# Optimization experiments

Measured on AMD Instinct MI355X. Metric: run time of the kernel, lower is better.

Reference implementation:

```python
import jax, jax.numpy as jnp
import numpy as np

HEADS = 12
DIM_HEAD = 64

def setup_inputs() -> dict:
    key = jax.random.key(0)
    ks = jax.random.split(key, 5)
    B, S, D = 4, 2048, 768
    s = 0.02
    return {
        "x": jax.random.normal(ks[0], (B, S, D), dtype=jnp.float32),
        "Wq": jax.random.normal(ks[1], (D, D), dtype=jnp.float32) * s,
        "Wk": jax.random.normal(ks[2], (D, D), dtype=jnp.float32) * s,
        "Wv": jax.random.normal(ks[3], (D, D), dtype=jnp.float32) * s,
        "Wo": jax.random.normal(ks[4], (D, D), dtype=jnp.float32) * s,
        "bo": jnp.zeros((D,), dtype=jnp.float32),
    }

def reference(x, Wq, Wk, Wv, Wo, bo):
    B, S, D = x.shape
    H, Dh = HEADS, DIM_HEAD
    scale = Dh ** -0.5
    # projections (torch Linear: x @ W^T)
    q = (x @ Wq.T).reshape(B, S, H, Dh).transpose(0, 2, 1, 3) * scale  # [B,H,S,Dh]
    k = (x @ Wk.T).reshape(B, S, H, Dh).transpose(0, 2, 1, 3)
    v = (x @ Wv.T).reshape(B, S, H, Dh).transpose(0, 2, 1, 3)
    sim = jnp.einsum("bhid,bhjd->bhij", q, k)  # [B,H,S,S]
    mask_value = -jnp.finfo(sim.dtype).max
    causal_mask = jnp.triu(jnp.ones((S, S), dtype=bool), k=1)
    sim = jnp.where(causal_mask, mask_value, sim)
    attn = jax.nn.softmax(sim, axis=-1)
    # dropout is identity in eval mode
    out = jnp.einsum("bhij,bhjd->bhid", attn, v)  # [B,H,S,Dh]
    out = out.transpose(0, 2, 1, 3).reshape(B, S, H * Dh)
    return out @ Wo.T + bo
```

## Files before the change

kernel.cpp:

```cpp
#include <hip/hip_runtime.h>
#include <stdint.h>

typedef unsigned short u16;
typedef __bf16 bf16x8 __attribute__((ext_vector_type(8)));
typedef float f32x4 __attribute__((ext_vector_type(4)));
typedef u16 u16x4 __attribute__((ext_vector_type(4)));
typedef u16 u16x8 __attribute__((ext_vector_type(8)));
typedef uint32_t u32x2 __attribute__((ext_vector_type(2)));

#define LDS_CAST(p) (reinterpret_cast<__attribute__((address_space(3))) uint32_t*>(reinterpret_cast<uintptr_t>(p)))
#define GLB_CAST(p) (reinterpret_cast<const __attribute__((address_space(1))) uint32_t*>(reinterpret_cast<uintptr_t>(p)))
#define GLOAD16(g, l) __builtin_amdgcn_global_load_lds(GLB_CAST(g), LDS_CAST(l), 16, 0, 0)
#define AS3U16(p) (reinterpret_cast<__attribute__((address_space(3))) u16*>(reinterpret_cast<uintptr_t>(p)))

__device__ __forceinline__ u16 f2bf(float f) {
    uint32_t u = __builtin_bit_cast(uint32_t, f);
    u += 0x7fffu + ((u >> 16) & 1u);
    return (u16)(u >> 16);
}
__device__ __forceinline__ u16 bfbits(float f) {
    return __builtin_bit_cast(u16, (__bf16)f);
}

__global__ void cast_all(const float* __restrict__ x,
                         const float* __restrict__ a, const float* __restrict__ b,
                         const float* __restrict__ c, const float* __restrict__ d,
                         u16* __restrict__ ox, u16* __restrict__ oa, u16* __restrict__ ob,
                         u16* __restrict__ oc, u16* __restrict__ od) {
    const int bid = blockIdx.x;
    const float* in;
    u16* out;
    int i;
    if (bid < 6144) {
        in = x; out = ox; i = bid * 256 + threadIdx.x;
    } else {
        const int zb = bid - 6144;
        const int z = zb / 576, lb = zb % 576;
        in = (z == 0) ? a : (z == 1) ? b : (z == 2) ? c : d;
        out = (z == 0) ? oa : (z == 1) ? ob : (z == 2) ? oc : od;
        i = lb * 256 + threadIdx.x;
    }
    float4 f = reinterpret_cast<const float4*>(in)[i];
    u16x4 o;
    o.x = f2bf(f.x); o.y = f2bf(f.y); o.z = f2bf(f.z); o.w = f2bf(f.w);
    reinterpret_cast<u16x4*>(out)[i] = o;
}

__global__ __launch_bounds__(256, 2) void gemm_qkv(
    const u16* __restrict__ X, const u16* __restrict__ Wq,
    const u16* __restrict__ Wk, const u16* __restrict__ Wv,
    u16* __restrict__ qo, u16* __restrict__ ko, u16* __restrict__ vTo)
{
    __shared__ u16 As[2][128 * 32];
    __shared__ u16 Bs[3][2][128 * 32];
    const int tid = threadIdx.x;
    const int lane = tid & 63;
    const int w = tid >> 6;
    const int lr = lane & 15, lg = lane >> 4;
    const int wrow = (w >> 1) * 64, wcol = (w & 1) * 64;

    const int lin = blockIdx.x + blockIdx.y * 6;
    const int xcd = lin & 7, idx = lin >> 3;
    const int prow = xcd * 8 + idx / 6;
    const int bxc = idx % 6;
    const int row0 = prow * 128, col0 = bxc * 128;

    f32x4 acc[3][4][4];
#pragma unroll
    for (int zz = 0; zz < 3; ++zz)
#pragma unroll
        for (int m = 0; m < 4; ++m)
#pragma unroll
            for (int n = 0; n < 4; ++n)
#pragma unroll
                for (int j = 0; j < 4; ++j) acc[zz][m][n][j] = 0.f;

#define QSTAGE(KT)                                                                                 \
    {                                                                                              \
        const int buf_ = (KT) & 1;                                                                 \
        _Pragma("unroll")                                                                          \
        for (int it = 0; it < 2; ++it) {                                                           \
            const int c = it * 256 + w * 64 + lane;                                                \
            const int row = c >> 2, c16 = c & 3;                                                   \
            const size_t go = (size_t)row * 768 + (KT) * 32 + c16 * 8;                             \
            const int lo = (it * 256 + w * 64) * 8;                                                \
            GLOAD16(X  + (size_t)row0 * 768 + go, &As[buf_][lo]);                                  \
            GLOAD16(Wq + (size_t)col0 * 768 + go, &Bs[0][buf_][lo]);                               \
            GLOAD16(Wk + (size_t)col0 * 768 + go, &Bs[1][buf_][lo]);                               \
            GLOAD16(Wv + (size_t)col0 * 768 + go, &Bs[2][buf_][lo]);                               \
        }                                                                                          \
    }

#define QSTEP(KT, VN, PF)                                                                          \
    {                                                                                              \
        if (PF) QSTAGE((KT) + 1);                                                                  \
        asm volatile("s_waitcnt vmcnt(" #VN ")" ::: "memory");                                     \
        __builtin_amdgcn_s_barrier();                                                              \
        const int cur_ = (KT) & 1;                                                                 \
        bf16x8 af[4];                                                                              \
        _Pragma("unroll")                                                                          \
        for (int m = 0; m < 4; ++m) af[m] = *(const bf16x8*)&As[cur_][(wrow + m * 16 + lr) * 32 + lg * 8]; \
        _Pragma("unroll")                                                                          \
        for (int zz = 0; zz < 3; ++zz) {                                                           \
            bf16x8 bfr[4];                                                                         \
            _Pragma("unroll")                                                                      \
            for (int n = 0; n < 4; ++n) bfr[n] = *(const bf16x8*)&Bs[zz][cur_][(wcol + n * 16 + lr) * 32 + lg * 8]; \
            _Pragma("unroll")                                                                      \
            for (int m = 0; m < 4; ++m)                                                            \
                _Pragma("unroll")                                                                  \
                for (int n = 0; n < 4; ++n)                                                        \
                    acc[zz][m][n] = __builtin_amdgcn_mfma_f32_16x16x32_bf16(af[m], bfr[n], acc[zz][m][n], 0, 0, 0); \
        }                                                                                          \
        asm volatile("s_waitcnt lgkmcnt(0)" ::: "memory");                                         \
        __builtin_amdgcn_sched_barrier(0);                                                         \
        __builtin_amdgcn_s_barrier();                                                              \
    }

    QSTAGE(0);
    for (int kt = 0; kt < 23; ++kt) QSTEP(kt, 8, true);
    QSTEP(23, 0, false);
#undef QSTEP
#undef QSTAGE

#pragma unroll
    for (int zz = 0; zz < 2; ++zz) {
        u16* outp = (zz == 0) ? qo : ko;
        const float scl = (zz == 0) ? 0.18033688011112042f : 1.0f;
#pragma unroll
        for (int n = 0; n < 4; ++n) {
            const int j = col0 + wcol + n * 16 + lr;
            const int h = j >> 6, dh = j & 63;
#pragma unroll
            for (int m = 0; m < 4; ++m)
#pragma unroll
                for (int r = 0; r < 4; ++r) {
                    const int i = row0 + wrow + m * 16 + lg * 4 + r;
                    const int b = i >> 11, s = i & 2047;
                    outp[(((size_t)b * 12 + h) * 2048 + s) * 64 + dh] = bfbits(acc[zz][m][n][r] * scl);
                }
        }
    }
    {
#pragma unroll
        for (int n = 0; n < 4; ++n) {
            const int j = col0 + wcol + n * 16 + lr;
            const int h = j >> 6, dh = j & 63;
#pragma unroll
            for (int m = 0; m < 4; ++m) {
                const int i0 = row0 + wrow + m * 16 + lg * 4;
                const int b = i0 >> 11, s0 = i0 & 2047;
                u16x4 pk;
#pragma unroll
                for (int r = 0; r < 4; ++r) pk[r] = bfbits(acc[2][m][n][r]);
                *(u16x4*)&vTo[(((size_t)b * 12 + h) * 64 + dh) * 2048 + s0] = pk;
            }
        }
    }
}

template<bool DIAG>
__device__ __forceinline__ void attn_step(
    const bf16x8* aq, f32x4* o, float* lrow,
    const u16* __restrict__ Ksb, const u16* __restrict__ Vsb, u16* __restrict__ PT,
    int kvb, int qg0, int lr, int lg)
{
    f32x4 sacc[4];
#pragma unroll
    for (int n = 0; n < 4; ++n)
#pragma unroll
        for (int j = 0; j < 4; ++j) sacc[n][j] = 0.f;
    __builtin_amdgcn_s_setprio(1);
#pragma unroll
    for (int kk = 0; kk < 2; ++kk)
#pragma unroll
        for (int n = 0; n < 4; ++n) {
            const int row = n * 16 + lr;
            const int p = (kk * 4 + lg) ^ (row & 7);
            bf16x8 bk = *(const bf16x8*)&Ksb[row * 64 + p * 8];
            sacc[n] = __builtin_amdgcn_mfma_f32_16x16x32_bf16(aq[kk], bk, sacc[n], 0, 0, 0);
        }
    __builtin_amdgcn_s_setprio(0);

    float pv[4][4];
#pragma unroll
    for (int r = 0; r < 4; ++r) {
        float ls = 0.f;
#pragma unroll
        for (int n = 0; n < 4; ++n) {
            float sv = sacc[n][r];
            if (DIAG && (kvb + n * 16 + lr) > qg0 + r) sv = -1e30f;
            const float e = __builtin_amdgcn_exp2f(sv);
            pv[r][n] = e;
            ls += e;
        }
        lrow[r] += ls;
    }

#pragma unroll
    for (int n = 0; n < 4; ++n) {
        u16x4 pk;
#pragma unroll
        for (int r = 0; r < 4; ++r) pk[r] = bfbits(pv[r][n]);
        *(u16x4*)&PT[(n * 16 + lr) * 16 + lg * 4] = pk;
    }

    u32x2 t0, t1, t2, t3;
    __attribute__((address_space(3))) u16* pb = AS3U16(PT) + lg * 128 + lr * 4;
    asm volatile("ds_read_b64_tr_b16 %0, %1" : "=v"(t0) : "v"(pb) : "memory");
    asm volatile("ds_read_b64_tr_b16 %0, %1 offset:128" : "=v"(t1) : "v"(pb) : "memory");
    asm volatile("ds_read_b64_tr_b16 %0, %1 offset:1024" : "=v"(t2) : "v"(pb) : "memory");
    asm volatile("ds_read_b64_tr_b16 %0, %1 offset:1152" : "=v"(t3) : "v"(pb) : "memory");
    asm volatile("s_waitcnt lgkmcnt(0)" ::: "memory");
    __builtin_amdgcn_sched_barrier(0);
    union { u32x2 h[2]; bf16x8 v; } ua, ub;
    ua.h[0] = t0; ua.h[1] = t1;
    ub.h[0] = t2; ub.h[1] = t3;
    const bf16x8 ap0 = ua.v, ap1 = ub.v;

    __builtin_amdgcn_s_setprio(1);
#pragma unroll
    for (int n = 0; n < 4; ++n) {
        const int rowv = n * 16 + lr;
        const int p0 = (0 + lg) ^ (rowv & 7);
        const int p1 = (4 + lg) ^ (rowv & 7);
        bf16x8 bv0 = *(const bf16x8*)&Vsb[rowv * 64 + p0 * 8];
        bf16x8 bv1 = *(const bf16x8*)&Vsb[rowv * 64 + p1 * 8];
        o[n] = __builtin_amdgcn_mfma_f32_16x16x32_bf16(ap0, bv0, o[n], 0, 0, 0);
        o[n] = __builtin_amdgcn_mfma_f32_16x16x32_bf16(ap1, bv1, o[n], 0, 0, 0);
    }
    __builtin_amdgcn_s_setprio(0);
}

__global__ __launch_bounds__(256) void attn_kernel(
    const u16* __restrict__ q, const u16* __restrict__ k,
    const u16* __restrict__ vT, u16* __restrict__ attn)
{
    __shared__ u16 Ks[2][64 * 64];
    __shared__ u16 Vs[2][64 * 64];
    __shared__ u16 Ps[4][64 * 16];

    const int lin = blockIdx.x + (blockIdx.y << 4);
    const int logi = (lin & 7) * 96 + (lin >> 3);
    const int pair = logi & 15, bh = logi >> 4;

    const int qA = pair, qB = 31 - pair;
    const int tid = threadIdx.x, lane = tid & 63, w = tid >> 6;
    const int lr = lane & 15, lg = lane >> 4;

    const u16* Kp = k + (size_t)bh * 2048 * 64;
    const u16* Vp = vT + (size_t)bh * 64 * 2048;

    const u16* QpA = q + ((size_t)bh * 2048 + qA * 64 + w * 16) * 64;
    const u16* QpB = q + ((size_t)bh * 2048 + qB * 64 + w * 16) * 64;
    bf16x8 aqA[2], aqB[2];
    aqA[0] = *(const bf16x8*)&QpA[lr * 64 + lg * 8];
    aqA[1] = *(const bf16x8*)&QpA[lr * 64 + 32 + lg * 8];
    aqB[0] = *(const bf16x8*)&QpB[lr * 64 + lg * 8];
    aqB[1] = *(const bf16x8*)&QpB[lr * 64 + 32 + lg * 8];

    f32x4 oA[4], oB[4];
    float lA[4], lB[4];
#pragma unroll
    for (int n = 0; n < 4; ++n)
#pragma unroll
        for (int j = 0; j < 4; ++j) { oA[n][j] = 0.f; oB[n][j] = 0.f; }
#pragma unroll
    for (int r = 0; r < 4; ++r) { lA[r] = 0.f; lB[r] = 0.f; }

#define STAGE(T, BUF)                                                                        \
    {                                                                                        \
        _Pragma("unroll")                                                                    \
        for (int it = 0; it < 2; ++it) {                                                     \
            const int c = it * 256 + w * 64 + lane;                                          \
            const int row = c >> 3, pc = c & 7;                                              \
            const int lc = pc ^ (row & 7);                                                   \
            GLOAD16(Kp + (size_t)((T) * 64 + row) * 64 + lc * 8, &Ks[BUF][(it * 256 + w * 64) * 8]); \
            GLOAD16(Vp + (size_t)row * 2048 + (T) * 64 + lc * 8, &Vs[BUF][(it * 256 + w * 64) * 8]); \
        }                                                                                    \
    }

    STAGE(0, 0);
    const int qg0A = qA * 64 + w * 16 + lg * 4;
    const int qg0B = qB * 64 + w * 16 + lg * 4;

    int t = 0;
    for (; t < qA; ++t) {
        const int cur = t & 1;
        __syncthreads();
        STAGE(t + 1, cur ^ 1);
        attn_step<false>(aqB, oB, lB, Ks[cur], Vs[cur], Ps[w], t * 64, qg0B, lr, lg);
        attn_step<false>(aqA, oA, lA, Ks[cur], Vs[cur], Ps[w], t * 64, qg0A, lr, lg);
    }
    {
        const int cur = t & 1;
        __syncthreads();
        STAGE(t + 1, cur ^ 1);
        attn_step<false>(aqB, oB, lB, Ks[cur], Vs[cur], Ps[w], t * 64, qg0B, lr, lg);
        attn_step<true >(aqA, oA, lA, Ks[cur], Vs[cur], Ps[w], t * 64, qg0A, lr, lg);
        ++t;
    }
    for (; t < qB; ++t) {
        const int cur = t & 1;
        __syncthreads();
        STAGE(t + 1, cur ^ 1);
        attn_step<false>(aqB, oB, lB, Ks[cur], Vs[cur], Ps[w], t * 64, qg0B, lr, lg);
    }
    {
        const int cur = t & 1;
        __syncthreads();
        attn_step<true >(aqB, oB, lB, Ks[cur], Vs[cur], Ps[w], t * 64, qg0B, lr, lg);
    }
#undef STAGE

#pragma unroll
    for (int r = 0; r < 4; ++r) {
#pragma unroll
        for (int off = 1; off < 16; off <<= 1) {
            lA[r] += __shfl_xor(lA[r], off);
            lB[r] += __shfl_xor(lB[r], off);
        }
        lA[r] = 1.f / lA[r];
        lB[r] = 1.f / lB[r];
    }

    const int b = bh / 12, h = bh - b * 12;
#pragma unroll
    for (int n = 0; n < 4; ++n)
#pragma unroll
        for (int r = 0; r < 4; ++r) {
            const int sA = qA * 64 + w * 16 + lg * 4 + r;
            const int sB = qB * 64 + w * 16 + lg * 4 + r;
            attn[((size_t)b * 2048 + sA) * 768 + h * 64 + n * 16 + lr] = bfbits(oA[n][r] * lA[r]);
            attn[((size_t)b * 2048 + sB) * 768 + h * 64 + n * 16 + lr] = bfbits(oB[n][r] * lB[r]);
        }
}

__global__ __launch_bounds__(256) void gemm_out(
    const u16* __restrict__ A, const u16* __restrict__ Wo,
    const float* __restrict__ bo, float* __restrict__ out)
{
    __shared__ u16 As[2][64 * 32];
    __shared__ u16 Bs[2][128 * 32];
    const int tid = threadIdx.x;
    const int lane = tid & 63;
    const int w = tid >> 6;
    const int lr = lane & 15, lg = lane >> 4;
    const int wrow = (w >> 1) * 32, wcol = (w & 1) * 64;

    const int lin = blockIdx.x + blockIdx.y * 6;
    const int xcd = lin & 7, idx = lin >> 3;
    const int prow = xcd * 16 + idx / 6;
    const int bxc = idx % 6;
    const int row0 = prow * 64, col0 = bxc * 128;

    f32x4 acc[2][4];
#pragma unroll
    for (int m = 0; m < 2; ++m)
#pragma unroll
        for (int n = 0; n < 4; ++n)
#pragma unroll
            for (int j = 0; j < 4; ++j) acc[m][n][j] = 0.f;

#define OSTAGE(KT)                                                                                 \
    {                                                                                              \
        const int buf_ = (KT) & 1;                                                                 \
        {                                                           \
            const int c = w * 64 + lane;                                                           \
            const int row = c >> 2, c16 = c & 3;                                                   \
            GLOAD16(A + (size_t)(row0 + row) * 768 + (KT) * 32 + c16 * 8, &As[buf_][c * 8]);       \
        }                                                                                          \
        _Pragma("unroll")                                                                          \
        for (int it = 0; it < 2; ++it) {                          \
            const int c = it * 256 + w * 64 + lane;                                                \
            const int row = c >> 2, c16 = c & 3;                                                   \
            GLOAD16(Wo + (size_t)(col0 + row) * 768 + (KT) * 32 + c16 * 8, &Bs[buf_][c * 8]);      \
        }                                                                                          \
    }

#define OSTEP(KT, VN, PF)                                                                          \
    {                                                                                              \
        if (PF) OSTAGE((KT) + 1);                                                                  \
        asm volatile("s_waitcnt vmcnt(" #VN ")" ::: "memory");                                     \
        __builtin_amdgcn_s_barrier();                                                              \
        const int cur_ = (KT) & 1;                                                                 \
        bf16x8 af[2], bfr[4];                                                                      \
        _Pragma("unroll")                                                                          \
        for (int m = 0; m < 2; ++m) af[m] = *(const bf16x8*)&As[cur_][(wrow + m * 16 + lr) * 32 + lg * 8]; \
        _Pragma("unroll")                                                                          \
        for (int n = 0; n < 4; ++n) bfr[n] = *(const bf16x8*)&Bs[cur_][(wcol + n * 16 + lr) * 32 + lg * 8]; \
        asm volatile("s_waitcnt lgkmcnt(0)" ::: "memory");                                         \
        __builtin_amdgcn_sched_barrier(0);                                                         \
        __builtin_amdgcn_s_barrier();                                                              \
        _Pragma("unroll")                                                                          \
        for (int m = 0; m < 2; ++m)                                                                \
            _Pragma("unroll")                                                                      \
            for (int n = 0; n < 4; ++n)                                                            \
                acc[m][n] = __builtin_amdgcn_mfma_f32_16x16x32_bf16(af[m], bfr[n], acc[m][n], 0, 0, 0); \
    }

    OSTAGE(0);
    for (int kt = 0; kt < 23; ++kt) OSTEP(kt, 3, true);
    OSTEP(23, 0, false);
#undef OSTEP
#undef OSTAGE

#pragma unroll
    for (int n = 0; n < 4; ++n) {
        const int j = col0 + wcol + n * 16 + lr;
        const float bj = bo[j];
#pragma unroll
        for (int m = 0; m < 2; ++m)
#pragma unroll
            for (int r = 0; r < 4; ++r) {
                const int i = row0 + wrow + m * 16 + lg * 4 + r;
                out[(size_t)i * 768 + j] = acc[m][n][r] + bj;
            }
    }
}

extern "C" void kernel_launch(void* const* d_in, const int* in_sizes, int n_in,
                              void* d_out, int out_size, void* d_ws, size_t ws_size,
                              hipStream_t stream) {
    const float* x  = (const float*)d_in[0];
    const float* Wq = (const float*)d_in[1];
    const float* Wk = (const float*)d_in[2];
    const float* Wv = (const float*)d_in[3];
    const float* Wo = (const float*)d_in[4];
    const float* bo = (const float*)d_in[5];
    float* out = (float*)d_out;

    const size_t NX = 6291456;
    const size_t NW = 589824;
    if (ws_size < (NX * 4 + NW * 4 + NX) * sizeof(u16)) return;
    u16* ws  = (u16*)d_ws;
    u16* xb  = ws;
    u16* wqb = xb  + NX;
    u16* wkb = wqb + NW;
    u16* wvb = wkb + NW;
    u16* wob = wvb + NW;
    u16* qb_ = wob + NW;
    u16* kb_ = qb_ + NX;
    u16* vtb = kb_ + NX;
    u16* ab_ = vtb + NX;

    cast_all<<<6144 + 2304, 256, 0, stream>>>(x, Wq, Wk, Wv, Wo, xb, wqb, wkb, wvb, wob);

    gemm_qkv<<<dim3(6, 64), 256, 0, stream>>>(xb, wqb, wkb, wvb, qb_, kb_, vtb);
    attn_kernel<<<dim3(16, 48), 256, 0, stream>>>(qb_, kb_, vtb, ab_);
    gemm_out<<<dim3(6, 128), 256, 0, stream>>>(ab_, wob, bo, out);
}
```

Measured before the change: 120.8 us.

## Stage K/V in 128-key chunks to halve block barriers in attention loop

The attention loop now loads two 64-key K/V tiles per stage into a doubled shared buffer and issues a __syncthreads plus prefetch only every other tile. This halves the number of block-wide barriers and batches more async global-to-LDS loads per stage, giving loads a longer window to overlap with compute. In exchange, K/V shared memory doubles to 64 KB plus P scratch, which may reduce how many blocks fit per CU. Prefetch indices are clamped to tile 31, so some blocks load redundant tiles near the end.

After: 137.5 us. 1.14x slower.

```diff
diff --git a/kernel.cpp b/kernel.cpp
--- a/kernel.cpp
+++ b/kernel.cpp
@@ -235,8 +235,8 @@
     const u16* __restrict__ q, const u16* __restrict__ k,
     const u16* __restrict__ vT, u16* __restrict__ attn)
 {
-    __shared__ u16 Ks[2][64 * 64];
-    __shared__ u16 Vs[2][64 * 64];
+    __shared__ u16 Ks[2][2][64 * 64];
+    __shared__ u16 Vs[2][2][64 * 64];
     __shared__ u16 Ps[4][64 * 16];
 
     const int lin = blockIdx.x + (blockIdx.y << 4);
@@ -267,50 +267,55 @@
 #pragma unroll
     for (int r = 0; r < 4; ++r) { lA[r] = 0.f; lB[r] = 0.f; }
 
-#define STAGE(T, BUF)                                                                        \
-    {                                                                                        \
-        _Pragma("unroll")                                                                    \
-        for (int it = 0; it < 2; ++it) {                                                     \
-            const int c = it * 256 + w * 64 + lane;                                          \
-            const int row = c >> 3, pc = c & 7;                                              \
-            const int lc = pc ^ (row & 7);                                                   \
-            GLOAD16(Kp + (size_t)((T) * 64 + row) * 64 + lc * 8, &Ks[BUF][(it * 256 + w * 64) * 8]); \
-            GLOAD16(Vp + (size_t)row * 2048 + (T) * 64 + lc * 8, &Vs[BUF][(it * 256 + w * 64) * 8]); \
-        }                                                                                    \
-    }
-
-    STAGE(0, 0);
+#define STAGE128(T, BUF)                                                                      \
+    {                                                                                         \
+        _Pragma("unroll")                                                                     \
+        for (int hh = 0; hh < 2; ++hh) {                                                      \
+            const int tt = ((T) + hh <= 31) ? (T) + hh : 31;                                  \
+            _Pragma("unroll")                                                                 \
+            for (int it = 0; it < 2; ++it) {                                                  \
+                const int c = it * 256 + w * 64 + lane;                                       \
+                const int row = c >> 3, pc = c & 7;                                           \
+                const int lc = pc ^ (row & 7);                                                \
+                GLOAD16(Kp + (size_t)(tt * 64 + row) * 64 + lc * 8, &Ks[BUF][hh][(it * 256 + w * 64) * 8]); \
+                GLOAD16(Vp + (size_t)row * 2048 + tt * 64 + lc * 8, &Vs[BUF][hh][(it * 256 + w * 64) * 8]); \
+            }                                                                                 \
+        }                                                                                     \
+    }
+
+#define TILE_CTL(T)                                                                           \
+    const int buf_ = ((T) >> 1) & 1, half_ = (T) & 1;                                         \
+    if (half_ == 0) {                                                                         \
+        __syncthreads();                                                                      \
+        if ((T) + 2 <= qB) STAGE128((T) + 2, buf_ ^ 1);                                       \
+    }
+
+    STAGE128(0, 0);
     const int qg0A = qA * 64 + w * 16 + lg * 4;
     const int qg0B = qB * 64 + w * 16 + lg * 4;
 
     int t = 0;
     for (; t < qA; ++t) {
-        const int cur = t & 1;
-        __syncthreads();
-        STAGE(t + 1, cur ^ 1);
-        attn_step<false>(aqB, oB, lB, Ks[cur], Vs[cur], Ps[w], t * 64, qg0B, lr, lg);
-        attn_step<false>(aqA, oA, lA, Ks[cur], Vs[cur], Ps[w], t * 64, qg0A, lr, lg);
+        TILE_CTL(t);
+        attn_step<false>(aqB, oB, lB, Ks[buf_][half_], Vs[buf_][half_], Ps[w], t * 64, qg0B, lr, lg);
+        attn_step<false>(aqA, oA, lA, Ks[buf_][half_], Vs[buf_][half_], Ps[w], t * 64, qg0A, lr, lg);
     }
     {
-        const int cur = t & 1;
-        __syncthreads();
-        STAGE(t + 1, cur ^ 1);
-        attn_step<false>(aqB, oB, lB, Ks[cur], Vs[cur], Ps[w], t * 64, qg0B, lr, lg);
-        attn_step<true >(aqA, oA, lA, Ks[cur], Vs[cur], Ps[w], t * 64, qg0A, lr, lg);
+        TILE_CTL(t);
+        attn_step<false>(aqB, oB, lB, Ks[buf_][half_], Vs[buf_][half_], Ps[w], t * 64, qg0B, lr, lg);
+        attn_step<true >(aqA, oA, lA, Ks[buf_][half_], Vs[buf_][half_], Ps[w], t * 64, qg0A, lr, lg);
         ++t;
     }
     for (; t < qB; ++t) {
-        const int cur = t & 1;
-        __syncthreads();
-        STAGE(t + 1, cur ^ 1);
-        attn_step<false>(aqB, oB, lB, Ks[cur], Vs[cur], Ps[w], t * 64, qg0B, lr, lg);
+        TILE_CTL(t);
+        attn_step<false>(aqB, oB, lB, Ks[buf_][half_], Vs[buf_][half_], Ps[w], t * 64, qg0B, lr, lg);
     }
     {
-        const int cur = t & 1;
-        __syncthreads();
-        attn_step<true >(aqB, oB, lB, Ks[cur], Vs[cur], Ps[w], t * 64, qg0B, lr, lg);
-    }
-#undef STAGE
+        TILE_CTL(t);
+        attn_step<true >(aqB, oB, lB, Ks[buf_][half_], Vs[buf_][half_], Ps[w], t * 64, qg0B, lr, lg);
+    }
+#undef TILE_CTL
+#undef STAGE128
 
 #pragma unroll
     for (int r = 0; r < 4; ++r) {
```
